# Kernel tuning notes

Measured on AMD Instinct MI355X. Metric: run time of the kernel, lower is better.

The kernel has to match this reference:

```python
import jax, jax.numpy as jnp
import numpy as np

HEAD_NUM = 12


def setup_inputs() -> dict:
    key = jax.random.key(0)
    k1, k2 = jax.random.split(key)
    B, S, D = 64, 512, 768
    x = jax.random.normal(k1, (B, S, D), dtype=jnp.float32)
    # attention probabilities for B*12 heads, [S, S]
    atten = jax.random.uniform(k2, (B * HEAD_NUM, S, S), dtype=jnp.float32)
    return {"x": x, "atten": atten, "index": 256}


def reference(x, atten, index):
    B, S, D = x.shape
    # mean attention over heads: [B*H, S, S] -> [B, S, S]
    avg_atten = atten.reshape(B, HEAD_NUM, S, S).mean(axis=1)
    # attended-by score per token: column sum minus the diagonal (self-attention)
    attended_by = avg_atten.sum(axis=1) - jnp.diagonal(avg_atten, axis1=1, axis2=2)  # [B, S]
    ab = attended_by[:, 1:]  # exclude CLS position 0; [B, S-1]

    # top (index-2) most-attended tokens (indices shifted +1 back to full seq coords)
    _, top_idx = jax.lax.top_k(ab, index - 2)
    top_idx = top_idx.astype(jnp.int32) + 1  # [B, index-2]
    cls = jnp.zeros((B, 1), dtype=jnp.int32)
    keep_idx = jnp.sort(jnp.concatenate([top_idx, cls], axis=1), axis=1)  # [B, index-1]
    extract = jnp.take_along_axis(x, keep_idx[:, :, None], axis=1)  # [B, index-1, D]

    # remaining (least-attended) tokens -> softmax-weighted mean into one token
    k_other = S - index + 1
    neg_vals, other_idx = jax.lax.top_k(-ab, k_other)  # smallest attended_by values
    w = jax.nn.softmax(-neg_vals, axis=1)[:, :, None]  # [B, k_other, 1]
    other_tokens = jnp.take_along_axis(x, (other_idx.astype(jnp.int32) + 1)[:, :, None], axis=1)
    weight_sum_token = jnp.mean(w * other_tokens, axis=1, keepdims=True)  # [B, 1, D]

    return jnp.concatenate([extract, weight_sum_token], axis=1)  # [B, index, D]
```

## Files before the change

### kernel.cpp

```cpp
#include <hip/hip_runtime.h>
#include <cstdint>

#define BATCH 64
#define SEQ   512
#define DIM   768
#define HEADS 12
#define KEEP  254
#define NOUT  256
#define KOTHER 257

__global__ void k1_colsum(const float* __restrict__ atten, float4* __restrict__ partial) {
    int bid = blockIdx.x;
    int t   = threadIdx.x;
    int bh  = bid >> 2;
    int row0 = (bid & 3) << 7;
    const float4* A4 = (const float4*)(atten + (size_t)bh * SEQ * SEQ);
    const float4* p  = A4 + (size_t)row0 * (SEQ / 4) + t;
    float4 s = {0.f, 0.f, 0.f, 0.f};
#pragma unroll 8
    for (int r = 0; r < 128; ++r) {
        float4 v = p[(size_t)r * (SEQ / 4)];
        s.x += v.x; s.y += v.y; s.z += v.z; s.w += v.w;
    }
    partial[(size_t)bid * (SEQ / 4) + t] = s;
}

__global__ void k2_reduce_diag(const float* __restrict__ partial,
                               const float* __restrict__ atten,
                               float* __restrict__ ab) {
    int b = blockIdx.x;
    int j = threadIdx.x;
    float s = 0.f;
#pragma unroll
    for (int c = 0; c < 48; ++c)
        s += partial[((size_t)(b * 48 + c)) * SEQ + j];
    float d = 0.f;
#pragma unroll
    for (int h = 0; h < HEADS; ++h)
        d += atten[((size_t)(b * HEADS + h)) * SEQ * SEQ + (size_t)j * (SEQ + 1)];
    ab[b * SEQ + j] = (s - d) / 12.0f;
}

__global__ void k3_select(const float* __restrict__ ab,
                          int* __restrict__ srcidx,
                          int* __restrict__ otheridx,
                          float* __restrict__ otherw) {
    __shared__ float sab[SEQ];
    __shared__ int   smask[SEQ];
    __shared__ float sred[SEQ];
    int b = blockIdx.x;
    int j = threadIdx.x;
    sab[j] = ab[b * SEQ + j];
    __syncthreads();
    float v = sab[j];
    int r = 0;
    if (j >= 1) {
        for (int k = 1; k < SEQ; ++k) {
            float u = sab[k];
            r += (u > v) || (u == v && k < j);
        }
    }
    int keep = (j >= 1) && (r < KEEP);
    smask[j] = keep;
    __syncthreads();
    int cnt = 0;
    for (int k = 1; k < j; ++k) cnt += smask[k];
    sred[j] = (j >= 1 && !keep) ? v : -3.4e38f;
    __syncthreads();
    for (int st = 256; st > 0; st >>= 1) {
        if (j < st) sred[j] = fmaxf(sred[j], sred[j + st]);
        __syncthreads();
    }
    float m = sred[0];
    __syncthreads();
    float e = (j >= 1 && !keep) ? expf(v - m) : 0.f;
    sred[j] = e;
    __syncthreads();
    for (int st = 256; st > 0; st >>= 1) {
        if (j < st) sred[j] += sred[j + st];
        __syncthreads();
    }
    float se = sred[0];
    if (j == 0) srcidx[b * NOUT] = 0;
    if (j >= 1) {
        if (keep) {
            srcidx[b * NOUT + 1 + cnt] = j;
        } else {
            int q = (j - 1) - cnt;
            otheridx[b * KOTHER + q] = j;
            otherw[b * KOTHER + q] = e / se;
        }
    }
}

__global__ void k4_out(const float* __restrict__ x,
                       const int* __restrict__ srcidx,
                       const int* __restrict__ otheridx,
                       const float* __restrict__ otherw,
                       float* __restrict__ out) {
    int blk = blockIdx.x;
    int b = blk >> 8;
    int p = blk & 255;
    int t = threadIdx.x;
    const float4* x4 = (const float4*)x;
    float4* o4 = (float4*)out;
    if (p < 255) {
        int j = srcidx[blk];
        o4[(size_t)blk * 192 + t] = x4[((size_t)b * SEQ + j) * 192 + t];
    } else {
        float4 acc = {0.f, 0.f, 0.f, 0.f};
        for (int q = 0; q < KOTHER; ++q) {
            int   j = otheridx[b * KOTHER + q];
            float w = otherw[b * KOTHER + q];
            float4 xv = x4[((size_t)b * SEQ + j) * 192 + t];
            acc.x += w * xv.x; acc.y += w * xv.y;
            acc.z += w * xv.z; acc.w += w * xv.w;
        }
        const float inv = 1.0f / 257.0f;
        float4 o = {acc.x * inv, acc.y * inv, acc.z * inv, acc.w * inv};
        o4[(size_t)blk * 192 + t] = o;
    }
}

extern "C" void kernel_launch(void* const* d_in, const int* in_sizes, int n_in,
                              void* d_out, int out_size, void* d_ws, size_t ws_size,
                              hipStream_t stream) {
    const float* x     = (const float*)d_in[0];
    const float* atten = (const float*)d_in[1];
    float* out = (float*)d_out;
    char* ws = (char*)d_ws;

    float* partial  = (float*)ws;
    float* ab       = (float*)(ws + 6291456);
    int*   srcidx   = (int*)(ws + 6291456 + 131072);
    int*   otheridx = (int*)(ws + 6291456 + 131072 + 65536);
    float* otherw   = (float*)(ws + 6291456 + 131072 + 65536 + 65792);

    k1_colsum<<<dim3(BATCH * HEADS * 4), dim3(128), 0, stream>>>(atten, (float4*)partial);
    k2_reduce_diag<<<dim3(BATCH), dim3(SEQ), 0, stream>>>(partial, atten, ab);
    k3_select<<<dim3(BATCH), dim3(SEQ), 0, stream>>>(ab, srcidx, otheridx, otherw);
    k4_out<<<dim3(BATCH * NOUT), dim3(192), 0, stream>>>(x, srcidx, otheridx, otherw, out);
}
```

Before: 1.226 ms.

## Fuse diag/select kernels, use wave intrinsics, split weighted sum, nontemporal loads

Merges the column-reduction/diagonal kernel with the selection kernel so the attended-by scores stay in shared memory. The rank count now reads shared memory as float4. The prefix count and max/sum reductions use ballot/popcount and wave shuffles instead of serial loops and tree reductions. The weighted-sum token is split across 8 chunk blocks per batch, with a new combine kernel to add the partials. The column-sum loads of the large attention tensor are marked nontemporal. This costs one extra launch and a workspace buffer in exchange for more parallelism in the tail work.

```diff
diff --git a/kernel.cpp b/kernel.cpp
--- a/kernel.cpp
+++ b/kernel.cpp
@@ -8,28 +8,39 @@
 #define KEEP  254
 #define NOUT  256
 #define KOTHER 257
+#define WCHUNK 8
 
-__global__ void k1_colsum(const float* __restrict__ atten, float4* __restrict__ partial) {
+typedef float vf4 __attribute__((ext_vector_type(4)));
+
+__global__ void k1_colsum(const float* __restrict__ atten, vf4* __restrict__ partial) {
     int bid = blockIdx.x;
     int t   = threadIdx.x;
     int bh  = bid >> 2;
     int row0 = (bid & 3) << 7;
-    const float4* A4 = (const float4*)(atten + (size_t)bh * SEQ * SEQ);
-    const float4* p  = A4 + (size_t)row0 * (SEQ / 4) + t;
-    float4 s = {0.f, 0.f, 0.f, 0.f};
+    const vf4* A4 = (const vf4*)(atten + (size_t)bh * SEQ * SEQ);
+    const vf4* p  = A4 + (size_t)row0 * (SEQ / 4) + t;
+    vf4 s = {0.f, 0.f, 0.f, 0.f};
 #pragma unroll 8
     for (int r = 0; r < 128; ++r) {
-        float4 v = p[(size_t)r * (SEQ / 4)];
+        vf4 v = __builtin_nontemporal_load(&p[(size_t)r * (SEQ / 4)]);
         s.x += v.x; s.y += v.y; s.z += v.z; s.w += v.w;
     }
     partial[(size_t)bid * (SEQ / 4) + t] = s;
 }
 
-__global__ void k2_reduce_diag(const float* __restrict__ partial,
-                               const float* __restrict__ atten,
-                               float* __restrict__ ab) {
+__global__ void k23_select(const float* __restrict__ partial,
+                           const float* __restrict__ atten,
+                           int* __restrict__ srcidx,
+                           int* __restrict__ otheridx,
+                           float* __restrict__ otherw) {
+    __shared__ __align__(16) float sab[SEQ];
+    __shared__ int   wsum[8];
+    __shared__ float wred[8];
     int b = blockIdx.x;
     int j = threadIdx.x;
+    int lane = j & 63;
+    int w = j >> 6;
+
     float s = 0.f;
 #pragma unroll
     for (int c = 0; c < 48; ++c)
@@ -38,49 +49,49 @@
 #pragma unroll
     for (int h = 0; h < HEADS; ++h)
         d += atten[((size_t)(b * HEADS + h)) * SEQ * SEQ + (size_t)j * (SEQ + 1)];
-    ab[b * SEQ + j] = (s - d) / 12.0f;
-}
+    float v = (s - d) / 12.0f;
+    sab[j] = v;
+    __syncthreads();
 
-__global__ void k3_select(const float* __restrict__ ab,
-                          int* __restrict__ srcidx,
-                          int* __restrict__ otheridx,
-                          float* __restrict__ otherw) {
-    __shared__ float sab[SEQ];
-    __shared__ int   smask[SEQ];
-    __shared__ float sred[SEQ];
-    int b = blockIdx.x;
-    int j = threadIdx.x;
-    sab[j] = ab[b * SEQ + j];
-    __syncthreads();
-    float v = sab[j];
     int r = 0;
     if (j >= 1) {
-        for (int k = 1; k < SEQ; ++k) {
-            float u = sab[k];
-            r += (u > v) || (u == v && k < j);
+#pragma unroll 4
+        for (int k4 = 0; k4 < SEQ; k4 += 4) {
+            float4 u = *(const float4*)&sab[k4];
+            r += (u.x > v) || (u.x == v && (k4 + 0) < j);
+            r += (u.y > v) || (u.y == v && (k4 + 1) < j);
+            r += (u.z > v) || (u.z == v && (k4 + 2) < j);
+            r += (u.w > v) || (u.w == v && (k4 + 3) < j);
         }
+        float u0 = sab[0];
+        r -= (u0 > v) || (u0 == v);
     }
     int keep = (j >= 1) && (r < KEEP);
-    smask[j] = keep;
+
+    unsigned long long m = __ballot(keep);
+    if (lane == 0) wsum[w] = (int)__popcll(m);
+    int cnt = __popcll(m & ((1ull << lane) - 1ull));
     __syncthreads();
-    int cnt = 0;
-    for (int k = 1; k < j; ++k) cnt += smask[k];
-    sred[j] = (j >= 1 && !keep) ? v : -3.4e38f;
+    for (int i = 0; i < w; ++i) cnt += wsum[i];
+
+    float ov = (j >= 1 && !keep) ? v : -3.4e38f;
+    for (int off = 32; off; off >>= 1) ov = fmaxf(ov, __shfl_xor(ov, off));
+    if (lane == 0) wred[w] = ov;
     __syncthreads();
-    for (int st = 256; st > 0; st >>= 1) {
-        if (j < st) sred[j] = fmaxf(sred[j], sred[j + st]);
-        __syncthreads();
-    }
-    float m = sred[0];
+    float mmax = wred[0];
+#pragma unroll
+    for (int i = 1; i < 8; ++i) mmax = fmaxf(mmax, wred[i]);
+
+    float e = (j >= 1 && !keep) ? expf(v - mmax) : 0.f;
+    float es = e;
+    for (int off = 32; off; off >>= 1) es += __shfl_xor(es, off);
     __syncthreads();
-    float e = (j >= 1 && !keep) ? expf(v - m) : 0.f;
-    sred[j] = e;
+    if (lane == 0) wred[w] = es;
     __syncthreads();
-    for (int st = 256; st > 0; st >>= 1) {
-        if (j < st) sred[j] += sred[j + st];
-        __syncthreads();
-    }
-    float se = sred[0];
+    float se = 0.f;
+#pragma unroll
+    for (int i = 0; i < 8; ++i) se += wred[i];
+
     if (j == 0) srcidx[b * NOUT] = 0;
     if (j >= 1) {
         if (keep) {
@@ -97,29 +108,48 @@
                        const int* __restrict__ srcidx,
                        const int* __restrict__ otheridx,
                        const float* __restrict__ otherw,
-                       float* __restrict__ out) {
+                       float* __restrict__ out,
+                       float* __restrict__ wpart) {
     int blk = blockIdx.x;
-    int b = blk >> 8;
-    int p = blk & 255;
     int t = threadIdx.x;
     const float4* x4 = (const float4*)x;
-    float4* o4 = (float4*)out;
-    if (p < 255) {
+    if (blk < BATCH * NOUT) {
+        int b = blk >> 8;
+        int p = blk & 255;
+        if (p == 255) return;
         int j = srcidx[blk];
-        o4[(size_t)blk * 192 + t] = x4[((size_t)b * SEQ + j) * 192 + t];
+        ((float4*)out)[(size_t)blk * 192 + t] = x4[((size_t)b * SEQ + j) * 192 + t];
     } else {
+        int widx = blk - BATCH * NOUT;
+        int b = widx >> 3;
+        int c = widx & 7;
+        int q0 = c ? 32 * c + 1 : 0;
+        int qn = c ? 32 : 33;
         float4 acc = {0.f, 0.f, 0.f, 0.f};
-        for (int q = 0; q < KOTHER; ++q) {
-            int   j = otheridx[b * KOTHER + q];
-            float w = otherw[b * KOTHER + q];
-            float4 xv = x4[((size_t)b * SEQ + j) * 192 + t];
-            acc.x += w * xv.x; acc.y += w * xv.y;
-            acc.z += w * xv.z; acc.w += w * xv.w;
+        for (int q = q0; q < q0 + qn; ++q) {
+            int   jj = otheridx[b * KOTHER + q];
+            float ww = otherw[b * KOTHER + q];
+            float4 xv = x4[((size_t)b * SEQ + jj) * 192 + t];
+            acc.x += ww * xv.x; acc.y += ww * xv.y;
+            acc.z += ww * xv.z; acc.w += ww * xv.w;
         }
-        const float inv = 1.0f / 257.0f;
-        float4 o = {acc.x * inv, acc.y * inv, acc.z * inv, acc.w * inv};
-        o4[(size_t)blk * 192 + t] = o;
+        ((float4*)wpart)[(size_t)widx * 192 + t] = acc;
     }
+}
+
+__global__ void k5_combine(const float* __restrict__ wpart, float* __restrict__ out) {
+    int b = blockIdx.x;
+    int t = threadIdx.x;
+    const float4* wp4 = (const float4*)wpart;
+    float4 a = {0.f, 0.f, 0.f, 0.f};
+#pragma unroll
+    for (int c = 0; c < WCHUNK; ++c) {
+        float4 v = wp4[((size_t)(b * WCHUNK + c)) * 192 + t];
+        a.x += v.x; a.y += v.y; a.z += v.z; a.w += v.w;
+    }
+    const float inv = 1.0f / 257.0f;
+    float4 o = {a.x * inv, a.y * inv, a.z * inv, a.w * inv};
+    ((float4*)out)[((size_t)(b * NOUT + 255)) * 192 + t] = o;
 }
 
 extern "C" void kernel_launch(void* const* d_in, const int* in_sizes, int n_in,
@@ -131,13 +161,14 @@
     char* ws = (char*)d_ws;
 
     float* partial  = (float*)ws;
-    float* ab       = (float*)(ws + 6291456);
-    int*   srcidx   = (int*)(ws + 6291456 + 131072);
-    int*   otheridx = (int*)(ws + 6291456 + 131072 + 65536);
-    float* otherw   = (float*)(ws + 6291456 + 131072 + 65536 + 65792);
+    int*   srcidx   = (int*)(ws + 6291456);
+    int*   otheridx = (int*)(ws + 6291456 + 65536);
+    float* otherw   = (float*)(ws + 6291456 + 65536 + 65792);
+    float* wpart    = (float*)(ws + 6291456 + 65536 + 65792 + 65792);
 
-    k1_colsum<<<dim3(BATCH * HEADS * 4), dim3(128), 0, stream>>>(atten, (float4*)partial);
-    k2_reduce_diag<<<dim3(BATCH), dim3(SEQ), 0, stream>>>(partial, atten, ab);
-    k3_select<<<dim3(BATCH), dim3(SEQ), 0, stream>>>(ab, srcidx, otheridx, otherw);
-    k4_out<<<dim3(BATCH * NOUT), dim3(192), 0, stream>>>(x, srcidx, otheridx, otherw, out);
+    k1_colsum<<<dim3(BATCH * HEADS * 4), dim3(128), 0, stream>>>(atten, (vf4*)partial);
+    k23_select<<<dim3(BATCH), dim3(SEQ), 0, stream>>>(partial, atten, srcidx, otheridx, otherw);
+    k4_out<<<dim3(BATCH * NOUT + BATCH * WCHUNK), dim3(192), 0, stream>>>(
+        x, srcidx, otheridx, otherw, out, wpart);
+    k5_combine<<<dim3(BATCH), dim3(192), 0, stream>>>(wpart, out);
 }
```

Result: faster. 1.091 ms (-11.0%).
